# Performance work log

Measured on AMD Instinct MI355X. Metric: run time of the kernel, lower is better.

## Reference

```python
import jax, jax.numpy as jnp
import numpy as np

EPSILON = 1e-9

def squash(s):
    # s: [..., K]; squash over last (capsule-dim) axis
    sq_norm = jnp.sum(s * s, axis=-1, keepdims=True)
    scale = sq_norm / (1.0 + sq_norm) / jnp.sqrt(sq_norm + EPSILON)
    return scale * s

def setup_inputs() -> dict:
    key = jax.random.key(0)
    k1, k2 = jax.random.split(key)
    B, Ni, Di = 256, 1152, 8   # batch, num input capsules, input capsule dim
    No, K = 10, 16             # num digit capsules, digit capsule dim
    x = jax.random.normal(k1, (B, Ni, Di), dtype=jnp.float32)
    # he_normal on fan_in = Di of the transformation matrices
    W = jax.random.normal(k2, (Ni, No, K, Di), dtype=jnp.float32) * np.sqrt(2.0 / Di)
    bias = jnp.zeros((No, K), dtype=jnp.float32)
    return {"x": x, "W": W, "bias": bias}

def reference(x, W, bias):
    routing_iterations = 3
    # u_hat[b,i,o,k] = sum_d W[i,o,k,d] * x[b,i,d]
    u_hat = jnp.einsum('bid,iokd->biok', x, W)  # [B, Ni, No, K]
    B, Ni, No, K = u_hat.shape
    b_logits = jnp.zeros((B, Ni, No), dtype=u_hat.dtype)
    v = None
    for i in range(routing_iterations):
        c = jax.nn.softmax(b_logits, axis=2)              # over output capsules
        s = jnp.einsum('bio,biok->bok', c, u_hat) + bias  # [B, No, K]
        v = squash(s)                                     # [B, No, K]
        if i < routing_iterations - 1:
            agreement = jnp.einsum('bok,biok->bio', v, u_hat)
            b_logits = b_logits + agreement
    return v
```

## Files before the change

kernel.cpp:

```cpp
#include <hip/hip_runtime.h>
#include <hip/hip_fp16.h>
#include <stdint.h>

#define NB 256
#define NI 1152
#define DI 8
#define NO 10
#define NK 16
#define NC 36
#define XPAD 10

#define WS_NEED 94371840ull

__global__ __launch_bounds__(320)
void uhat_kernel(const float* __restrict__ x, const float* __restrict__ W,
                 uint32_t* __restrict__ ws)
{
    __shared__ float x_lds[16 * 32 * XPAD];

    const int c   = blockIdx.x;
    const int b0  = blockIdx.y * 16;
    const int tid = threadIdx.x;
    const int o   = tid >> 5;
    const int il  = tid & 31;

    for (int idx = tid; idx < 16 * 256; idx += 320) {
        const int bb = idx >> 8, r = idx & 255;
        x_lds[bb * (32 * XPAD) + (r >> 3) * XPAD + (r & 7)] =
            x[(size_t)(b0 + bb) * (NI * DI) + c * 256 + r];
    }
    __syncthreads();

    const int i = c * 32 + il;
    const float4* wp = reinterpret_cast<const float4*>(W + ((size_t)i * NO + o) * (NK * DI));

#pragma unroll
    for (int h = 0; h < 2; ++h) {
        float4 wr[16];
#pragma unroll
        for (int t = 0; t < 16; ++t) wr[t] = wp[h * 16 + t];

        for (int bb = 0; bb < 16; ++bb) {
            const float2* xp = reinterpret_cast<const float2*>(
                &x_lds[bb * (32 * XPAD) + il * XPAD]);
            const float2 x01 = xp[0], x23 = xp[1], x45 = xp[2], x67 = xp[3];

            float u[8];
#pragma unroll
            for (int kk = 0; kk < 8; ++kk) {
                const float4 w0 = wr[2 * kk], w1 = wr[2 * kk + 1];
                u[kk] = w0.x * x01.x + w0.y * x01.y + w0.z * x23.x + w0.w * x23.y +
                        w1.x * x45.x + w1.y * x45.y + w1.z * x67.x + w1.w * x67.y;
            }

            uint32_t pk[4];
#pragma unroll
            for (int t = 0; t < 4; ++t) {
                union { __half2 h2; uint32_t w; } cv;
                cv.h2 = __float22half2_rn(make_float2(u[2 * t], u[2 * t + 1]));
                pk[t] = cv.w;
            }
            const size_t base =
                ((((size_t)(b0 + bb) * NC + c) * 2 + h) * NO + o) * 128 + il * 4;
            *reinterpret_cast<uint4*>(ws + base) = make_uint4(pk[0], pk[1], pk[2], pk[3]);
        }
    }
}

#define BW    12
#define BSTEP 12

__global__ __launch_bounds__(768)
void route_kernel(const float* __restrict__ bias, float* __restrict__ out,
                  const uint32_t* __restrict__ ws)
{
    __shared__ float v_lds[NO * NK];
    __shared__ float s_red[BW][NO * NK];
    __shared__ float blog_lds[NI * 11];

    const int tid = threadIdx.x;
    const int b   = blockIdx.x;
    const int w   = tid >> 6;
    const int l   = tid & 63;
    const int ii  = l >> 3;
    const int k2  = l & 7;
    const int k0  = k2 * 2;
    const int h   = k2 >> 2;
    const int k2q = k2 & 3;

    const uint32_t* ub = ws + (size_t)b * 92160 + h * 1280 + k2q;
    const int ibase = w * 96;

    float s0a[NO], s1a[NO];

#pragma unroll
    for (int o = 0; o < NO; ++o) { s0a[o] = 0.f; s1a[o] = 0.f; }

    for (int s = 0; s < BSTEP; ++s) {
        const int i = ibase + s * 8 + ii;
        const uint32_t* up = ub + (i >> 5) * 2560 + (i & 31) * 4;
#pragma unroll
        for (int o = 0; o < NO; ++o) {
            union { uint32_t u; __half2 h2; } cv; cv.u = up[o * 128];
            const float2 f = __half22float2(cv.h2);
            s0a[o] += f.x; s1a[o] += f.y;
        }
    }
#pragma unroll
    for (int m = 8; m <= 32; m <<= 1)
#pragma unroll
        for (int o = 0; o < NO; ++o) {
            s0a[o] += __shfl_xor(s0a[o], m, 64);
            s1a[o] += __shfl_xor(s1a[o], m, 64);
        }
    if (ii == 0) {
#pragma unroll
        for (int o = 0; o < NO; ++o) {
            s_red[w][o * NK + k0]     = s0a[o];
            s_red[w][o * NK + k0 + 1] = s1a[o];
        }
    }
    __syncthreads();
    if (tid < NO * NK) {
        float acc = 0.f;
#pragma unroll
        for (int ww = 0; ww < BW; ++ww) acc += s_red[ww][tid];
        const float sv = 0.1f * acc + bias[tid];
        float sq = sv * sv;
#pragma unroll
        for (int m = 8; m >= 1; m >>= 1) sq += __shfl_xor(sq, m, 64);
        const float scale = sq / (1.f + sq) / sqrtf(sq + 1e-9f);
        v_lds[tid] = scale * sv;
    }
    __syncthreads();

    for (int it = 0; it < 2; ++it) {
        float vk0[NO], vk1[NO];
#pragma unroll
        for (int o = 0; o < NO; ++o) {
            vk0[o] = v_lds[o * NK + k0];
            vk1[o] = v_lds[o * NK + k0 + 1];
        }
#pragma unroll
        for (int o = 0; o < NO; ++o) { s0a[o] = 0.f; s1a[o] = 0.f; }

        uint32_t uu[NO];
        {
            const int i0 = ibase + ii;
            const uint32_t* up = ub + (i0 >> 5) * 2560 + (i0 & 31) * 4;
#pragma unroll
            for (int o = 0; o < NO; ++o) uu[o] = up[o * 128];
        }

        for (int s = 0; s < BSTEP; ++s) {
            const int i = ibase + s * 8 + ii;

            float fx[NO], fy[NO];
#pragma unroll
            for (int o = 0; o < NO; ++o) {
                union { uint32_t u; __half2 h2; } cv; cv.u = uu[o];
                const float2 f = __half22float2(cv.h2);
                fx[o] = f.x; fy[o] = f.y;
            }
            if (s + 1 < BSTEP) {
                const int i2 = ibase + (s + 1) * 8 + ii;
                const uint32_t* up2 = ub + (i2 >> 5) * 2560 + (i2 & 31) * 4;
#pragma unroll
                for (int o = 0; o < NO; ++o) uu[o] = up2[o * 128];
            }

            float a[NO];
#pragma unroll
            for (int o = 0; o < NO; ++o) a[o] = vk0[o] * fx[o] + vk1[o] * fy[o];
#pragma unroll
            for (int m = 1; m <= 4; m <<= 1)
#pragma unroll
                for (int o = 0; o < NO; ++o) a[o] += __shfl_xor(a[o], m, 64);

            const int row = i * 11;
            float tot[NO];
            if (it == 0) {
#pragma unroll
                for (int o = 0; o < NO; ++o) tot[o] = a[o];
                float w0v = 0.f, w1v = 0.f;
#pragma unroll
                for (int o = 0; o < 8; ++o) if (k2 == o) w0v = a[o];
#pragma unroll
                for (int o = 0; o < 2; ++o) if (k2 == o) w1v = a[8 + o];
                blog_lds[row + k2] = w0v;
                if (k2 < 2) blog_lds[row + 8 + k2] = w1v;
            } else {
#pragma unroll
                for (int o = 0; o < NO; ++o) tot[o] = blog_lds[row + o] + a[o];
            }

            float e[NO], den = 0.f;
#pragma unroll
            for (int o = 0; o < NO; ++o) { e[o] = __expf(tot[o]); den += e[o]; }
            const float rden = 1.f / den;
#pragma unroll
            for (int o = 0; o < NO; ++o) {
                const float cc = e[o] * rden;
                s0a[o] += cc * fx[o];
                s1a[o] += cc * fy[o];
            }
        }

#pragma unroll
        for (int m = 8; m <= 32; m <<= 1)
#pragma unroll
            for (int o = 0; o < NO; ++o) {
                s0a[o] += __shfl_xor(s0a[o], m, 64);
                s1a[o] += __shfl_xor(s1a[o], m, 64);
            }
        if (ii == 0) {
#pragma unroll
            for (int o = 0; o < NO; ++o) {
                s_red[w][o * NK + k0]     = s0a[o];
                s_red[w][o * NK + k0 + 1] = s1a[o];
            }
        }
        __syncthreads();

        if (tid < NO * NK) {
            float sv = bias[tid];
#pragma unroll
            for (int ww = 0; ww < BW; ++ww) sv += s_red[ww][tid];
            float sq = sv * sv;
#pragma unroll
            for (int m = 8; m >= 1; m >>= 1) sq += __shfl_xor(sq, m, 64);
            const float scale = sq / (1.f + sq) / sqrtf(sq + 1e-9f);
            if (it == 1) out[(size_t)b * (NO * NK) + tid] = scale * sv;
            else         v_lds[tid] = scale * sv;
        }
        __syncthreads();
    }
}

__device__ __forceinline__ void compute_uhat_fb(int i, int o,
        const float* x_lds, const float* __restrict__ W, float* u)
{
    float xr[DI];
#pragma unroll
    for (int d = 0; d < DI; ++d) xr[d] = x_lds[i * 9 + d];
    const float4* wp = reinterpret_cast<const float4*>(W + (size_t)(i * NO + o) * (NK * DI));
#pragma unroll
    for (int k = 0; k < NK; ++k) {
        float4 w0 = wp[2 * k], w1 = wp[2 * k + 1];
        u[k] = w0.x * xr[0] + w0.y * xr[1] + w0.z * xr[2] + w0.w * xr[3] +
               w1.x * xr[4] + w1.y * xr[5] + w1.z * xr[6] + w1.w * xr[7];
    }
}

__global__ __launch_bounds__(640)
void digitcaps_fallback(const float* __restrict__ x, const float* __restrict__ W,
                        const float* __restrict__ bias, float* __restrict__ out)
{
    __shared__ float x_lds[NI * 9];
    __shared__ float blog_lds[64][NO + 1];
    __shared__ float v_lds[NO][NK];
    const int b = blockIdx.x, tid = threadIdx.x;
    const int o = tid >> 6, il = tid & 63;
    const float* xb = x + (size_t)b * (NI * DI);
    for (int idx = tid; idx < NI * DI; idx += 640)
        x_lds[(idx >> 3) * 9 + (idx & 7)] = xb[idx];
    float bias_r[NK];
#pragma unroll
    for (int k = 0; k < NK; ++k) bias_r[k] = bias[o * NK + k];
    __syncthreads();
    float blog[18], s_acc[NK];
    auto finish = [&](int it) {
#pragma unroll
        for (int off = 32; off >= 1; off >>= 1)
#pragma unroll
            for (int k = 0; k < NK; ++k) s_acc[k] += __shfl_xor(s_acc[k], off, 64);
        float sv[NK], sq = 0.f;
#pragma unroll
        for (int k = 0; k < NK; ++k) { sv[k] = s_acc[k] + bias_r[k]; sq += sv[k] * sv[k]; }
        const float scale = sq / (1.f + sq) / sqrtf(sq + 1e-9f);
        if (il == 0) {
            if (it == 2) {
#pragma unroll
                for (int k = 0; k < NK; ++k) out[(size_t)b * 160 + o * NK + k] = scale * sv[k];
            } else {
#pragma unroll
                for (int k = 0; k < NK; ++k) v_lds[o][k] = scale * sv[k];
            }
        }
    };
#pragma unroll
    for (int k = 0; k < NK; ++k) s_acc[k] = 0.f;
    for (int c = 0; c < 18; ++c) {
        float u[NK];
        compute_uhat_fb(c * 64 + il, o, x_lds, W, u);
#pragma unroll
        for (int k = 0; k < NK; ++k) s_acc[k] += u[k];
        blog[c] = 0.f;
    }
#pragma unroll
    for (int k = 0; k < NK; ++k) s_acc[k] *= 0.1f;
    finish(0);
    __syncthreads();
    for (int it = 1; it <= 2; ++it) {
#pragma unroll
        for (int k = 0; k < NK; ++k) s_acc[k] = 0.f;
        for (int c = 0; c < 18; ++c) {
            const int i = c * 64 + il;
            float u[NK];
            compute_uhat_fb(i, o, x_lds, W, u);
            float a = 0.f;
#pragma unroll
            for (int k = 0; k < NK; ++k) a += v_lds[o][k] * u[k];
            blog[c] += a;
            __syncthreads();
            blog_lds[il][o] = blog[c];
            __syncthreads();
            float m = blog_lds[il][0];
#pragma unroll
            for (int oo = 1; oo < NO; ++oo) m = fmaxf(m, blog_lds[il][oo]);
            float den = 0.f;
#pragma unroll
            for (int oo = 0; oo < NO; ++oo) den += __expf(blog_lds[il][oo] - m);
            const float cv = __expf(blog[c] - m) / den;
#pragma unroll
            for (int k = 0; k < NK; ++k) s_acc[k] += cv * u[k];
        }
        finish(it);
        __syncthreads();
    }
}

extern "C" void kernel_launch(void* const* d_in, const int* in_sizes, int n_in,
                              void* d_out, int out_size, void* d_ws, size_t ws_size,
                              hipStream_t stream)
{
    const float* x    = (const float*)d_in[0];
    const float* W    = (const float*)d_in[1];
    const float* bias = (const float*)d_in[2];
    float* out = (float*)d_out;

    if (ws_size >= WS_NEED) {
        uhat_kernel<<<dim3(NC, 16), 320, 0, stream>>>(x, W, (uint32_t*)d_ws);
        route_kernel<<<NB, 768, 0, stream>>>(bias, out, (const uint32_t*)d_ws);
    } else {
        digitcaps_fallback<<<NB, 640, 0, stream>>>(x, W, bias, out);
    }
}
```

Before: 145.7 us.

## Compute first-iteration routing partial sums in u_hat kernel epilogue

```diff
diff --git a/kernel.cpp b/kernel.cpp
--- a/kernel.cpp
+++ b/kernel.cpp
@@ -10,7 +10,8 @@
 #define NC 36
 #define XPAD 10
 
-#define WS_NEED 94371840ull
+#define PART_OFF_U32 23592960u
+#define WS_NEED ((23592960ull + 1474560ull) * 4ull)
 
 __global__ __launch_bounds__(320)
 void uhat_kernel(const float* __restrict__ x, const float* __restrict__ W,
@@ -64,6 +65,34 @@
                 ((((size_t)(b0 + bb) * NC + c) * 2 + h) * NO + o) * 128 + il * 4;
             *reinterpret_cast<uint4*>(ws + base) = make_uint4(pk[0], pk[1], pk[2], pk[3]);
         }
+    }
+
+    __syncthreads();
+
+    const int bq = tid / 80;
+    const int r2 = tid - bq * 80;
+    const int po = r2 >> 3;
+    const int k2 = r2 & 7;
+    const int ph = k2 >> 2;
+    const int pq = k2 & 3;
+
+    float* partw = reinterpret_cast<float*>(ws + PART_OFF_U32);
+
+#pragma unroll
+    for (int t = 0; t < 4; ++t) {
+        const int bb = bq + t * 4;
+        const int b  = b0 + bb;
+        const uint32_t* up = ws +
+            (((size_t)b * NC + c) * 2 + ph) * 1280 + po * 128 + pq;
+        float accx = 0.f, accy = 0.f;
+#pragma unroll 8
+        for (int il2 = 0; il2 < 32; ++il2) {
+            union { uint32_t u; __half2 h2; } cv; cv.u = up[il2 * 4];
+            const float2 f = __half22float2(cv.h2);
+            accx += f.x; accy += f.y;
+        }
+        float* pp = partw + (((size_t)c * NB + b) * NO + po) * NK + k2 * 2;
+        pp[0] = accx; pp[1] = accy;
     }
 }
 
@@ -88,44 +117,16 @@
     const int h   = k2 >> 2;
     const int k2q = k2 & 3;
 
-    const uint32_t* ub = ws + (size_t)b * 92160 + h * 1280 + k2q;
+    const uint32_t* ub = ws + (size_t)b * 92160u + h * 1280 + k2q;
     const int ibase = w * 96;
 
-    float s0a[NO], s1a[NO];
-
-#pragma unroll
-    for (int o = 0; o < NO; ++o) { s0a[o] = 0.f; s1a[o] = 0.f; }
-
-    for (int s = 0; s < BSTEP; ++s) {
-        const int i = ibase + s * 8 + ii;
-        const uint32_t* up = ub + (i >> 5) * 2560 + (i & 31) * 4;
-#pragma unroll
-        for (int o = 0; o < NO; ++o) {
-            union { uint32_t u; __half2 h2; } cv; cv.u = up[o * 128];
-            const float2 f = __half22float2(cv.h2);
-            s0a[o] += f.x; s1a[o] += f.y;
-        }
-    }
-#pragma unroll
-    for (int m = 8; m <= 32; m <<= 1)
-#pragma unroll
-        for (int o = 0; o < NO; ++o) {
-            s0a[o] += __shfl_xor(s0a[o], m, 64);
-            s1a[o] += __shfl_xor(s1a[o], m, 64);
-        }
-    if (ii == 0) {
-#pragma unroll
-        for (int o = 0; o < NO; ++o) {
-            s_red[w][o * NK + k0]     = s0a[o];
-            s_red[w][o * NK + k0 + 1] = s1a[o];
-        }
-    }
-    __syncthreads();
     if (tid < NO * NK) {
-        float acc = 0.f;
-#pragma unroll
-        for (int ww = 0; ww < BW; ++ww) acc += s_red[ww][tid];
-        const float sv = 0.1f * acc + bias[tid];
+        const float* part = reinterpret_cast<const float*>(ws + PART_OFF_U32);
+        float sv = 0.f;
+#pragma unroll 6
+        for (int cc = 0; cc < NC; ++cc)
+            sv += part[((size_t)cc * NB + b) * (NO * NK) + tid];
+        sv = 0.1f * sv + bias[tid];
         float sq = sv * sv;
 #pragma unroll
         for (int m = 8; m >= 1; m >>= 1) sq += __shfl_xor(sq, m, 64);
@@ -133,6 +134,8 @@
         v_lds[tid] = scale * sv;
     }
     __syncthreads();
+
+    float s0a[NO], s1a[NO];
 
     for (int it = 0; it < 2; ++it) {
         float vk0[NO], vk1[NO];
```

New measurement: 157.3 us. 8.0% more time.
